# Optimization experiments

Hardware: AMD Instinct MI355X
Metric: run time of the kernel (lower is better)

The kernel has to match this reference:

```python
import jax, jax.numpy as jnp
import numpy as np

LAM = 0.9
Z_MAX = 5.0


def setup_inputs() -> dict:
    key = jax.random.key(0)
    d2 = jax.random.uniform(key, (32, 2048, 512), dtype=jnp.float32)
    return {"d2": d2}


def reference(d2):
    # d2: (B, L, K). Leaky-integrator (EMA) over time with clamp to [0, Z_MAX].
    B, L, K = d2.shape
    one_minus = 1.0 - LAM

    def step(z_t, d2_t):
        z_t = jnp.clip(LAM * z_t + one_minus * d2_t, 0.0, Z_MAX)
        return z_t, z_t

    z0 = jnp.zeros((B, K), dtype=d2.dtype)
    # scan over time axis: move L to leading axis
    _, z = jax.lax.scan(step, z0, jnp.moveaxis(d2, 1, 0))
    return jnp.moveaxis(z, 0, 1)  # (B, L, K)
```

## Files before the change

kernel.cpp:

```cpp
#include <hip/hip_runtime.h>


constexpr int B  = 32;
constexpr int L  = 2048;
constexpr int K  = 512;
constexpr int NC = 8;
constexpr int C  = L / NC;
constexpr int W  = 64;

__global__ __launch_bounds__(256)
void ema_chunk_kernel(const float* __restrict__ d2, float* __restrict__ out) {
    const float lam = 0.9f, om = 0.1f, zmax = 5.0f;

    int tid = blockIdx.x * blockDim.x + threadIdx.x;
    int k   = tid & (K - 1);
    int bc  = tid >> 9;
    int c   = bc & (NC - 1);
    int b   = bc >> 3;

    const float* in = d2  + (size_t)b * L * K + k;
    float*       o  = out + (size_t)b * L * K + k;

    int t0 = c * C;
    int tw = t0 - W;
    if (tw < 0) tw = 0;

    float z = 0.0f;

    #pragma unroll 8
    for (int t = tw; t < t0; ++t) {
        float d = in[(size_t)t * K];
        z = fminf(fmaxf(lam * z + om * d, 0.0f), zmax);
    }

    #pragma unroll 8
    for (int t = t0; t < t0 + C; ++t) {
        float d = in[(size_t)t * K];
        z = fminf(fmaxf(lam * z + om * d, 0.0f), zmax);
        o[(size_t)t * K] = z;
    }
}

extern "C" void kernel_launch(void* const* d_in, const int* in_sizes, int n_in,
                              void* d_out, int out_size, void* d_ws, size_t ws_size,
                              hipStream_t stream) {
    const float* d2 = (const float*)d_in[0];
    float* out = (float*)d_out;

    int total = B * NC * K;
    int block = 256;
    int grid  = total / block;
    ema_chunk_kernel<<<grid, block, 0, stream>>>(d2, out);
}
```

Before: 49.14 us.

## Vectorize EMA scan to float4 with finer time chunks and nontemporal stores

Each thread now carries four adjacent channels through the scan using 16-byte loads and stores, and output is written with nontemporal stores. The time axis is split into 16 chunks instead of 8, so the warm-up window becomes a larger share of each chunk's reads. The aim is fewer, wider memory transactions and less cache pollution from output writes. In exchange, total threads halve and redundant warm-up traffic rises, which matters for a kernel that is already bandwidth-bound.

```diff
diff --git a/kernel.cpp b/kernel.cpp
--- a/kernel.cpp
+++ b/kernel.cpp
@@ -1,54 +1,64 @@
 #include <hip/hip_runtime.h>
 
+
+typedef float f32x4 __attribute__((ext_vector_type(4)));
 
 constexpr int B  = 32;
 constexpr int L  = 2048;
 constexpr int K  = 512;
-constexpr int NC = 8;
+constexpr int KV = K / 4;
+constexpr int NC = 16;
 constexpr int C  = L / NC;
 constexpr int W  = 64;
 
 __global__ __launch_bounds__(256)
-void ema_chunk_kernel(const float* __restrict__ d2, float* __restrict__ out) {
+void ema_chunk_v4_kernel(const f32x4* __restrict__ d2, f32x4* __restrict__ out) {
     const float lam = 0.9f, om = 0.1f, zmax = 5.0f;
 
     int tid = blockIdx.x * blockDim.x + threadIdx.x;
-    int k   = tid & (K - 1);
-    int bc  = tid >> 9;
+    int k4  = tid & (KV - 1);
+    int bc  = tid >> 7;
     int c   = bc & (NC - 1);
-    int b   = bc >> 3;
+    int b   = bc >> 4;
 
-    const float* in = d2  + (size_t)b * L * K + k;
-    float*       o  = out + (size_t)b * L * K + k;
+    const f32x4* in = d2  + (size_t)b * L * KV + k4;
+    f32x4*       o  = out + (size_t)b * L * KV + k4;
 
     int t0 = c * C;
     int tw = t0 - W;
     if (tw < 0) tw = 0;
 
-    float z = 0.0f;
+    float z0 = 0.0f, z1 = 0.0f, z2 = 0.0f, z3 = 0.0f;
 
     #pragma unroll 8
     for (int t = tw; t < t0; ++t) {
-        float d = in[(size_t)t * K];
-        z = fminf(fmaxf(lam * z + om * d, 0.0f), zmax);
+        f32x4 d = in[(size_t)t * KV];
+        z0 = fminf(fmaxf(lam * z0 + om * d.x, 0.0f), zmax);
+        z1 = fminf(fmaxf(lam * z1 + om * d.y, 0.0f), zmax);
+        z2 = fminf(fmaxf(lam * z2 + om * d.z, 0.0f), zmax);
+        z3 = fminf(fmaxf(lam * z3 + om * d.w, 0.0f), zmax);
     }
 
     #pragma unroll 8
     for (int t = t0; t < t0 + C; ++t) {
-        float d = in[(size_t)t * K];
-        z = fminf(fmaxf(lam * z + om * d, 0.0f), zmax);
-        o[(size_t)t * K] = z;
+        f32x4 d = in[(size_t)t * KV];
+        z0 = fminf(fmaxf(lam * z0 + om * d.x, 0.0f), zmax);
+        z1 = fminf(fmaxf(lam * z1 + om * d.y, 0.0f), zmax);
+        z2 = fminf(fmaxf(lam * z2 + om * d.z, 0.0f), zmax);
+        z3 = fminf(fmaxf(lam * z3 + om * d.w, 0.0f), zmax);
+        f32x4 r = {z0, z1, z2, z3};
+        __builtin_nontemporal_store(r, &o[(size_t)t * KV]);
     }
 }
 
 extern "C" void kernel_launch(void* const* d_in, const int* in_sizes, int n_in,
                               void* d_out, int out_size, void* d_ws, size_t ws_size,
                               hipStream_t stream) {
-    const float* d2 = (const float*)d_in[0];
-    float* out = (float*)d_out;
+    const f32x4* d2 = (const f32x4*)d_in[0];
+    f32x4* out = (f32x4*)d_out;
 
-    int total = B * NC * K;
+    int total = B * NC * KV;
     int block = 256;
     int grid  = total / block;
-    ema_chunk_kernel<<<grid, block, 0, stream>>>(d2, out);
+    ema_chunk_v4_kernel<<<grid, block, 0, stream>>>(d2, out);
 }
```

New measurement: 54.44 us. 10.8% more time.
